# Kernel optimization log

Hardware: AMD Instinct MI355X
Metric: run time of the kernel (lower is better)

## Reference

```python
import jax, jax.numpy as jnp
import numpy as np

B, E, D, H, NH, HD = 2, 1024, 1024, 2048, 16, 128
NEG = -1e9  # stands in for float('-inf') in the torch mask; same softmax result


def _rotate_half(x):
    x1, x2 = x[..., : x.shape[-1] // 2], x[..., x.shape[-1] // 2 :]
    return jnp.concatenate((-x2, x1), axis=-1)


def setup_inputs() -> dict:
    key = jax.random.key(0)
    ks = jax.random.split(key, 8)
    hidden_states = jax.random.normal(ks[0], (B, D, H), dtype=jnp.float32)
    encoder_states = jax.random.normal(ks[1], (B, E, H), dtype=jnp.float32)
    # RoPE tables for the decoder positions
    inv_freq = 1.0 / (10000.0 ** (jnp.arange(0, HD, 2, dtype=jnp.float32) / HD))
    pos = jnp.arange(D, dtype=jnp.float32)
    freqs = pos[:, None] * inv_freq[None, :]            # [D, HD/2]
    emb = jnp.concatenate([freqs, freqs], axis=-1)      # [D, HD]
    cos = jnp.broadcast_to(jnp.cos(emb)[None], (B, D, HD)).astype(jnp.float32)
    sin = jnp.broadcast_to(jnp.sin(emb)[None], (B, D, HD)).astype(jnp.float32)
    # causal dec-dec mask [B,1,D,D]
    tri = jnp.tril(jnp.ones((D, D), dtype=bool))
    attention_mask = jnp.where(tri, 0.0, NEG).astype(jnp.float32)[None, None]
    attention_mask = jnp.broadcast_to(attention_mask, (B, 1, D, D))
    std = 0.02
    Wq = jax.random.normal(ks[2], (H, H), dtype=jnp.float32) * std
    Wk = jax.random.normal(ks[3], (H, H), dtype=jnp.float32) * std
    Wv = jax.random.normal(ks[4], (H, H), dtype=jnp.float32) * std
    Wo = jax.random.normal(ks[5], (H, H), dtype=jnp.float32) * std
    return {
        "hidden_states": hidden_states,
        "encoder_states": encoder_states,
        "cos": cos,
        "sin": sin,
        "attention_mask": attention_mask,
        "Wq": Wq,
        "Wk": Wk,
        "Wv": Wv,
        "Wo": Wo,
    }


def reference(hidden_states, encoder_states, cos, sin, attention_mask, Wq, Wk, Wv, Wo):
    b, d, h = hidden_states.shape
    e = encoder_states.shape[1]
    s = e + d
    scaling = HD ** -0.5
    # build concatenated enc/dec mask [B,1,S,S]
    enc_enc = jnp.zeros((b, 1, e, e), dtype=hidden_states.dtype)
    enc_dec = jnp.full((b, 1, e, d), NEG, dtype=hidden_states.dtype)
    dec_enc = jnp.zeros((b, 1, d, e), dtype=hidden_states.dtype)
    upper = jnp.concatenate([enc_enc, enc_dec], axis=-1)
    lower = jnp.concatenate([dec_enc, attention_mask], axis=-1)
    full_mask = jnp.concatenate([upper, lower], axis=-2)  # [B,1,S,S]

    hs = jnp.concatenate([encoder_states, hidden_states], axis=1)  # [B,S,H]
    def proj(W):
        return jnp.einsum("bsh,oh->bso", hs, W).reshape(b, s, NH, HD).transpose(0, 2, 1, 3)
    q, k, v = proj(Wq), proj(Wk), proj(Wv)  # [B,NH,S,HD]

    # partial RoPE: only on decoder slice
    c = cos[:, None]  # [B,1,D,HD]
    si = sin[:, None]
    q_dec = q[:, :, e:] * c + _rotate_half(q[:, :, e:]) * si
    k_dec = k[:, :, e:] * c + _rotate_half(k[:, :, e:]) * si
    q = jnp.concatenate([q[:, :, :e], q_dec], axis=2)
    k = jnp.concatenate([k[:, :, :e], k_dec], axis=2)

    scores = jnp.einsum("bhqd,bhkd->bhqk", q, k) * scaling + full_mask
    attn = jax.nn.softmax(scores.astype(jnp.float32), axis=-1).astype(q.dtype)
    out = jnp.einsum("bhqk,bhkd->bhqd", attn, v)            # [B,NH,S,HD]
    out = out.transpose(0, 2, 1, 3).reshape(b, s, NH * HD)   # [B,S,H]
    out = jnp.einsum("bsh,oh->bso", out, Wo)
    out = out[:, -d:, :]  # keep decoder outputs only
    return out, attn
```

## Files before the change

### kernel.cpp

```cpp
#include <hip/hip_runtime.h>
#include <cstdint>
#include <cstddef>

typedef _Float16 f16;
typedef __attribute__((ext_vector_type(8))) _Float16 half8;
typedef __attribute__((ext_vector_type(4))) float f32x4;

constexpr int Bb = 2, Ee = 1024, Dd = 1024, Hh = 2048, NHh = 16, HDd = 128, Ss = 2048;
constexpr float SCALE = 0.08838834764831845f;
constexpr int PSTR = 84;

#define DEVINL __device__ __forceinline__
#define GLD_LDS(gp, lp) \
  __builtin_amdgcn_global_load_lds((const __attribute__((address_space(1))) void*)(gp), \
                                   (__attribute__((address_space(3))) void*)(lp), 16, 0, 0)

DEVINL f16 f2h(float x) { return (f16)x; }
DEVINL float h2f(f16 x) { return (float)x; }

__global__ void convert_hs_k(const float* __restrict__ hid, const float* __restrict__ enc,
                             f16* __restrict__ dst) {
  size_t idx = ((size_t)blockIdx.x * 256 + threadIdx.x) * 8;
  int b = (int)(idx >> 22);
  size_t r = idx & ((1ull << 22) - 1);
  int s = (int)(r >> 11);
  int hc = (int)(r & 2047);
  const float* src = (s < Ee) ? (enc + (((size_t)b * Ee + s) << 11) + hc)
                              : (hid + (((size_t)b * Dd + (s - Ee)) << 11) + hc);
  float4 x0 = *(const float4*)src;
  float4 x1 = *(const float4*)(src + 4);
  union { f16 u[8]; uint4 v; } o;
  o.u[0] = f2h(x0.x); o.u[1] = f2h(x0.y); o.u[2] = f2h(x0.z); o.u[3] = f2h(x0.w);
  o.u[4] = f2h(x1.x); o.u[5] = f2h(x1.y); o.u[6] = f2h(x1.z); o.u[7] = f2h(x1.w);
  *(uint4*)(dst + idx) = o.v;
}

__global__ void convert_w_k(const float* __restrict__ w0, const float* __restrict__ w1,
                            const float* __restrict__ w2, const float* __restrict__ w3,
                            f16* __restrict__ dst) {
  const float* srcs[4] = {w0, w1, w2, w3};
  int z = blockIdx.y;
  size_t idx = ((size_t)blockIdx.x * 256 + threadIdx.x) * 8;
  const float* s = srcs[z] + idx;
  f16* d = dst + (size_t)z * Hh * Hh + idx;
  float4 x0 = *(const float4*)s;
  float4 x1 = *(const float4*)(s + 4);
  union { f16 u[8]; uint4 v; } o;
  o.u[0] = f2h(x0.x); o.u[1] = f2h(x0.y); o.u[2] = f2h(x0.z); o.u[3] = f2h(x0.w);
  o.u[4] = f2h(x1.x); o.u[5] = f2h(x1.y); o.u[6] = f2h(x1.z); o.u[7] = f2h(x1.w);
  *(uint4*)d = o.v;
}

template <int MODE>
__global__ __launch_bounds__(256) void gemm_k(const f16* __restrict__ A,
                                              const f16* __restrict__ Bw,
                                              void* __restrict__ Cout) {
  __shared__ f16 Alds[128 * 64];
  __shared__ f16 Blds[128 * 64];
  const int tid = threadIdx.x;
  const int lane = tid & 63, w = tid >> 6;
  const int lr = lane & 15, lq = lane >> 4;
  const int m0 = blockIdx.y * 128, n0 = blockIdx.x * 128;
  const int wm = (w >> 1) * 64, wn = (w & 1) * 64;
  f32x4 acc[4][4] = {};

  for (int k0 = 0; k0 < 2048; k0 += 64) {
    __syncthreads();
#pragma unroll
    for (int t = 0; t < 4; ++t) {
      int c = t * 256 + tid;
      int row = c >> 3, cof = (c & 7) << 3;
      const f16* ga = A + ((size_t)(m0 + row) << 11) + k0 + cof;
      const f16* gb = Bw + ((size_t)(n0 + row) << 11) + k0 + cof;
      int lo = (t * 256 + w * 64) * 8;
      GLD_LDS(ga, Alds + lo);
      GLD_LDS(gb, Blds + lo);
    }
    __syncthreads();
#pragma unroll
    for (int kk = 0; kk < 2; ++kk) {
      half8 af[4], bf[4];
#pragma unroll
      for (int i = 0; i < 4; ++i) {
        af[i] = *(const half8*)(Alds + (wm + i * 16 + lr) * 64 + kk * 32 + lq * 8);
        bf[i] = *(const half8*)(Blds + (wn + i * 16 + lr) * 64 + kk * 32 + lq * 8);
      }
#pragma unroll
      for (int i = 0; i < 4; ++i)
#pragma unroll
        for (int j = 0; j < 4; ++j)
          acc[i][j] = __builtin_amdgcn_mfma_f32_16x16x32_f16(af[i], bf[j], acc[i][j], 0, 0, 0);
    }
  }

#pragma unroll
  for (int i = 0; i < 4; ++i) {
#pragma unroll
    for (int j = 0; j < 4; ++j) {
      const int col = n0 + wn + j * 16 + lr;
#pragma unroll
      for (int jj = 0; jj < 4; ++jj) {
        const int row = m0 + wm + i * 16 + lq * 4 + jj;
        float v = acc[i][j][jj];
        if constexpr (MODE == 2) {
          ((float*)Cout)[((size_t)row << 11) + col] = v;
        } else {
          const int bb = row >> 11, s = row & 2047;
          const int hh = col >> 7, hd = col & 127;
          size_t o;
          if constexpr (MODE == 0)
            o = ((((size_t)bb * NHh + hh) * Ss + s) << 7) + hd;
          else
            o = ((((size_t)bb * NHh + hh) * HDd + hd) << 11) + s;
          ((f16*)Cout)[o] = f2h(v);
        }
      }
    }
  }
}

__global__ void rope_k(f16* __restrict__ q, f16* __restrict__ k,
                       const float* __restrict__ cosp, const float* __restrict__ sinp) {
  size_t idx = (size_t)blockIdx.x * 256 + threadIdx.x;
  const int d = (int)(idx & 63);
  const int sdec = (int)((idx >> 6) & 1023);
  const int h = (int)((idx >> 16) & 15);
  const int b = (int)(idx >> 20);
  const size_t base = (((size_t)b * NHh + h) * Ss + Ee + sdec) * HDd;
  const size_t cbase = ((size_t)b * Dd + sdec) * HDd;
  const float c1 = cosp[cbase + d], s1 = sinp[cbase + d];
  const float c2 = cosp[cbase + d + 64], s2 = sinp[cbase + d + 64];
  {
    float x1 = h2f(q[base + d]), x2 = h2f(q[base + d + 64]);
    q[base + d] = f2h(x1 * c1 - x2 * s1);
    q[base + d + 64] = f2h(x2 * c2 + x1 * s2);
  }
  {
    float x1 = h2f(k[base + d]), x2 = h2f(k[base + d + 64]);
    k[base + d] = f2h(x1 * c1 - x2 * s1);
    k[base + d + 64] = f2h(x2 * c2 + x1 * s2);
  }
}

__global__ __launch_bounds__(256) void attn_k(const f16* __restrict__ qw,
                                              const f16* __restrict__ kw,
                                              const f16* __restrict__ vw,
                                              float* __restrict__ attn,
                                              f16* __restrict__ ctx) {
  __shared__ f16 KV[2][8192];
  __shared__ f16 Plds[4][16 * PSTR];
  const int tid = threadIdx.x;
  const int lane = tid & 63, w = tid >> 6;
  const int lr = lane & 15, lq = lane >> 4;

  const int n = blockIdx.x;
  const int orig = (n & 7) * 128 + (n >> 3);
  const int qt = orig & 31;
  const int h = (orig >> 5) & 15;
  const int b = orig >> 9;
  const int q0 = (31 - qt) * 64;
  const bool dec = q0 >= Ee;
  const int kt_lim = dec ? (q0 / 64 + 1) : (Ee / 64);
  const size_t bh = (size_t)b * NHh + h;

#define STAGE_K(dst, kt_)                                                        \
  {                                                                              \
    _Pragma("unroll") for (int t = 0; t < 4; ++t) {                              \
      int c = t * 256 + tid;                                                     \
      int row = c >> 4;                                                          \
      int gs = (c & 15) ^ (row & 7);                                             \
      GLD_LDS(kw + (bh * Ss + (kt_) * 64 + row) * HDd + gs * 8, (dst) + c * 8);  \
    }                                                                            \
  }
#define STAGE_V(dst, kt_)                                                        \
  {                                                                              \
    _Pragma("unroll") for (int t = 0; t < 4; ++t) {                              \
      int c = t * 256 + tid;                                                     \
      int row = c >> 3;                                                          \
      int gs = (c & 7) ^ (row & 7);                                              \
      GLD_LDS(vw + (bh * HDd + row) * Ss + (kt_) * 64 + gs * 8, (dst) + c * 8);  \
    }                                                                            \
  }

  const f16* qbase = qw + (bh * Ss + q0 + w * 16 + lr) * HDd + lq * 8;
  half8 aq[4];
#pragma unroll
  for (int kk = 0; kk < 4; ++kk) aq[kk] = *(const half8*)(qbase + kk * 32);

  const int qrow_base = q0 + w * 16 + lq * 4;
  float lsum[4] = {0.f, 0.f, 0.f, 0.f};

  STAGE_K(KV[0], 0);
  __syncthreads();
  int cur = 0;
  for (int kt = 0; kt < kt_lim; ++kt) {
    if (kt + 1 < kt_lim) STAGE_K(KV[cur ^ 1], kt + 1);
    const f16* Kp = KV[cur];
#pragma unroll
    for (int j = 0; j < 4; ++j) {
      f32x4 sc = {0.f, 0.f, 0.f, 0.f};
#pragma unroll
      for (int kk = 0; kk < 4; ++kk) {
        half8 bk = *(const half8*)(Kp + (j * 16 + lr) * 128 + (((kk << 2) + lq) ^ (lr & 7)) * 8);
        sc = __builtin_amdgcn_mfma_f32_16x16x32_f16(aq[kk], bk, sc, 0, 0, 0);
      }
      const int col = kt * 64 + j * 16 + lr;
#pragma unroll
      for (int jj = 0; jj < 4; ++jj) {
        bool masked = dec && col >= Ee && col > qrow_base + jj;
        lsum[jj] += masked ? 0.f : __expf(sc[jj] * SCALE);
      }
    }
    __syncthreads();
    cur ^= 1;
  }
#pragma unroll
  for (int jj = 0; jj < 4; ++jj) {
#pragma unroll
    for (int o = 1; o < 16; o <<= 1) lsum[jj] += __shfl_xor(lsum[jj], o);
  }
  float rl[4];
#pragma unroll
  for (int jj = 0; jj < 4; ++jj) rl[jj] = 1.f / lsum[jj];

  f32x4 accv[8] = {};

  for (int kt = 0; kt < kt_lim; ++kt) {
    __syncthreads();
    STAGE_K(KV[0], kt);
    if (dec) STAGE_V(KV[1], kt);
    __syncthreads();
#pragma unroll
    for (int j = 0; j < 4; ++j) {
      f32x4 sc = {0.f, 0.f, 0.f, 0.f};
#pragma unroll
      for (int kk = 0; kk < 4; ++kk) {
        half8 bk = *(const half8*)(KV[0] + (j * 16 + lr) * 128 + (((kk << 2) + lq) ^ (lr & 7)) * 8);
        sc = __builtin_amdgcn_mfma_f32_16x16x32_f16(aq[kk], bk, sc, 0, 0, 0);
      }
      const int col = kt * 64 + j * 16 + lr;
#pragma unroll
      for (int jj = 0; jj < 4; ++jj) {
        const int qrow = qrow_base + jj;
        bool masked = dec && col >= Ee && col > qrow;
        float p = masked ? 0.f : __expf(sc[jj] * SCALE) * rl[jj];
        __builtin_nontemporal_store(p, &attn[(bh * Ss + qrow) * (size_t)Ss + col]);
        if (dec) Plds[w][(lq * 4 + jj) * PSTR + j * 16 + lr] = f2h(p);
      }
    }
    if (dec) {
#pragma unroll
      for (int kk2 = 0; kk2 < 2; ++kk2) {
        half8 ap = *(const half8*)(&Plds[w][lr * PSTR + kk2 * 32 + lq * 8]);
#pragma unroll
        for (int nt = 0; nt < 8; ++nt) {
          half8 bv = *(const half8*)(KV[1] + (nt * 16 + lr) * 64 + (((kk2 << 2) + lq) ^ (lr & 7)) * 8);
          accv[nt] = __builtin_amdgcn_mfma_f32_16x16x32_f16(ap, bv, accv[nt], 0, 0, 0);
        }
      }
    }
  }

  {
    const int zc0 = kt_lim * 64;
    const int Z = Ss - zc0;
    if (Z > 0) {
      const int per_row = Z >> 2;
      for (int idx = tid; idx < 64 * per_row; idx += 256) {
        int r = idx / per_row;
        int cc = (idx - r * per_row) << 2;
        f32x4 z = {0.f, 0.f, 0.f, 0.f};
        __builtin_nontemporal_store(z, (f32x4*)(attn + (bh * Ss + q0 + r) * (size_t)Ss + zc0 + cc));
      }
    }
  }

  if (dec) {
#pragma unroll
    for (int nt = 0; nt < 8; ++nt)
#pragma unroll
      for (int jj = 0; jj < 4; ++jj) {
        int sd = qrow_base + jj - Ee;
        ctx[((size_t)b * Dd + sd) * Hh + h * HDd + nt * 16 + lr] = f2h(accv[nt][jj]);
      }
  }
#undef STAGE_K
#undef STAGE_V
}

extern "C" void kernel_launch(void* const* d_in, const int* in_sizes, int n_in,
                              void* d_out, int out_size, void* d_ws, size_t ws_size,
                              hipStream_t stream) {
  const float* hidden  = (const float*)d_in[0];
  const float* encoder = (const float*)d_in[1];
  const float* cosp    = (const float*)d_in[2];
  const float* sinp    = (const float*)d_in[3];
  const float* Wq = (const float*)d_in[5];
  const float* Wk = (const float*)d_in[6];
  const float* Wv = (const float*)d_in[7];
  const float* Wo = (const float*)d_in[8];

  f16* ws = (f16*)d_ws;
  size_t off = 0;
  f16* hs_f = ws + off; off += (size_t)Bb * Ss * Hh;
  f16* W_f  = ws + off; off += (size_t)4 * Hh * Hh;
  f16* q_f  = ws + off; off += (size_t)Bb * NHh * Ss * HDd;
  f16* k_f  = ws + off; off += (size_t)Bb * NHh * Ss * HDd;
  f16* v_f  = ws + off; off += (size_t)Bb * NHh * Ss * HDd;
  f16* ctx_f = ws + off; off += (size_t)Bb * Dd * Hh;

  float* outp = (float*)d_out;
  float* attnp = outp + (size_t)Bb * Dd * Hh;

  convert_hs_k<<<4096, 256, 0, stream>>>(hidden, encoder, hs_f);
  convert_w_k<<<dim3(2048, 4), 256, 0, stream>>>(Wq, Wk, Wv, Wo, W_f);
  gemm_k<0><<<dim3(16, 32), 256, 0, stream>>>(hs_f, W_f + 0 * (size_t)Hh * Hh, q_f);
  gemm_k<0><<<dim3(16, 32), 256, 0, stream>>>(hs_f, W_f + 1 * (size_t)Hh * Hh, k_f);
  gemm_k<1><<<dim3(16, 32), 256, 0, stream>>>(hs_f, W_f + 2 * (size_t)Hh * Hh, v_f);
  rope_k<<<8192, 256, 0, stream>>>(q_f, k_f, cosp, sinp);
  attn_k<<<1024, 256, 0, stream>>>(q_f, k_f, v_f, attnp, ctx_f);
  gemm_k<2><<<dim3(16, 16), 256, 0, stream>>>(ctx_f, W_f + 3 * (size_t)Hh * Hh, outp);
}
```

Measured before the change: 442.8 us.

## Double-buffer K/V in attention pass two, stage attn stores via LDS, batch QKV GEMMs

The second attention pass now double-buffers K and V tiles in separate LDS buffers, so the next tile's global-to-LDS loads overlap the current tile's compute instead of being fenced by two barriers per iteration. Softmax probabilities are written to the per-wave P buffer for every block, then read back so each lane stores 16 contiguous floats of the attention matrix, replacing scattered scalar stores. The three QKV projection GEMMs are merged into one launch using grid z. In exchange, LDS use roughly doubles, which may lower occupancy. The stored attention weights are now rounded through fp16, which costs some precision.

```diff
diff --git a/kernel.cpp b/kernel.cpp
--- a/kernel.cpp
+++ b/kernel.cpp
@@ -8,7 +8,7 @@
 
 constexpr int Bb = 2, Ee = 1024, Dd = 1024, Hh = 2048, NHh = 16, HDd = 128, Ss = 2048;
 constexpr float SCALE = 0.08838834764831845f;
-constexpr int PSTR = 84;
+constexpr int PSTR = 88;
 
 #define DEVINL __device__ __forceinline__
 #define GLD_LDS(gp, lp) \
@@ -51,10 +51,76 @@
   *(uint4*)d = o.v;
 }
 
-template <int MODE>
-__global__ __launch_bounds__(256) void gemm_k(const f16* __restrict__ A,
-                                              const f16* __restrict__ Bw,
-                                              void* __restrict__ Cout) {
+__global__ __launch_bounds__(256) void gemm_qkv_k(const f16* __restrict__ A,
+                                                  const f16* __restrict__ W,
+                                                  f16* __restrict__ qo,
+                                                  f16* __restrict__ ko,
+                                                  f16* __restrict__ vo) {
+  __shared__ f16 Alds[128 * 64];
+  __shared__ f16 Blds[128 * 64];
+  const int tid = threadIdx.x;
+  const int lane = tid & 63, w = tid >> 6;
+  const int lr = lane & 15, lq = lane >> 4;
+  const int m0 = blockIdx.y * 128, n0 = blockIdx.x * 128;
+  const int z = blockIdx.z;
+  const f16* Bw = W + (size_t)z * Hh * Hh;
+  const int wm = (w >> 1) * 64, wn = (w & 1) * 64;
+  f32x4 acc[4][4] = {};
+
+  for (int k0 = 0; k0 < 2048; k0 += 64) {
+    __syncthreads();
+#pragma unroll
+    for (int t = 0; t < 4; ++t) {
+      int c = t * 256 + tid;
+      int row = c >> 3, cof = (c & 7) << 3;
+      const f16* ga = A + ((size_t)(m0 + row) << 11) + k0 + cof;
+      const f16* gb = Bw + ((size_t)(n0 + row) << 11) + k0 + cof;
+      int lo = (t * 256 + w * 64) * 8;
+      GLD_LDS(ga, Alds + lo);
+      GLD_LDS(gb, Blds + lo);
+    }
+    __syncthreads();
+#pragma unroll
+    for (int kk = 0; kk < 2; ++kk) {
+      half8 af[4], bf[4];
+#pragma unroll
+      for (int i = 0; i < 4; ++i) {
+        af[i] = *(const half8*)(Alds + (wm + i * 16 + lr) * 64 + kk * 32 + lq * 8);
+        bf[i] = *(const half8*)(Blds + (wn + i * 16 + lr) * 64 + kk * 32 + lq * 8);
+      }
+#pragma unroll
+      for (int i = 0; i < 4; ++i)
+#pragma unroll
+        for (int j = 0; j < 4; ++j)
+          acc[i][j] = __builtin_amdgcn_mfma_f32_16x16x32_f16(af[i], bf[j], acc[i][j], 0, 0, 0);
+    }
+  }
+
+  f16* out = (z == 0) ? qo : (z == 1) ? ko : vo;
+#pragma unroll
+  for (int i = 0; i < 4; ++i) {
+#pragma unroll
+    for (int j = 0; j < 4; ++j) {
+      const int col = n0 + wn + j * 16 + lr;
+      const int hh = col >> 7, hd = col & 127;
+#pragma unroll
+      for (int jj = 0; jj < 4; ++jj) {
+        const int row = m0 + wm + i * 16 + lq * 4 + jj;
+        const int bb = row >> 11, s = row & 2047;
+        size_t o;
+        if (z < 2)
+          o = ((((size_t)bb * NHh + hh) * Ss + s) << 7) + hd;
+        else
+          o = ((((size_t)bb * NHh + hh) * HDd + hd) << 11) + s;
+        out[o] = f2h(acc[i][j][jj]);
+      }
+    }
+  }
+}
+
+__global__ __launch_bounds__(256) void gemm_out_k(const f16* __restrict__ A,
+                                                  const f16* __restrict__ Bw,
+                                                  float* __restrict__ Cout) {
   __shared__ f16 Alds[128 * 64];
   __shared__ f16 Blds[128 * 64];
   const int tid = threadIdx.x;
@@ -94,29 +160,16 @@
   }
 
 #pragma unroll
-  for (int i = 0; i < 4; ++i) {
+  for (int i = 0; i < 4; ++i)
 #pragma unroll
     for (int j = 0; j < 4; ++j) {
       const int col = n0 + wn + j * 16 + lr;
 #pragma unroll
       for (int jj = 0; jj < 4; ++jj) {
         const int row = m0 + wm + i * 16 + lq * 4 + jj;
-        float v = acc[i][j][jj];
-        if constexpr (MODE == 2) {
-          ((float*)Cout)[((size_t)row << 11) + col] = v;
-        } else {
-          const int bb = row >> 11, s = row & 2047;
-          const int hh = col >> 7, hd = col & 127;
-          size_t o;
-          if constexpr (MODE == 0)
-            o = ((((size_t)bb * NHh + hh) * Ss + s) << 7) + hd;
-          else
-            o = ((((size_t)bb * NHh + hh) * HDd + hd) << 11) + s;
-          ((f16*)Cout)[o] = f2h(v);
-        }
-      }
-    }
-  }
+        Cout[((size_t)row << 11) + col] = acc[i][j][jj];
+      }
+    }
 }
 
 __global__ void rope_k(f16* __restrict__ q, f16* __restrict__ k,
@@ -147,7 +200,8 @@
                                               const f16* __restrict__ vw,
                                               float* __restrict__ attn,
                                               f16* __restrict__ ctx) {
-  __shared__ f16 KV[2][8192];
+  __shared__ f16 Kb[2][8192];
+  __shared__ f16 Vb[2][8192];
   __shared__ f16 Plds[4][16 * PSTR];
   const int tid = threadIdx.x;
   const int lane = tid & 63, w = tid >> 6;
@@ -190,12 +244,12 @@
   const int qrow_base = q0 + w * 16 + lq * 4;
   float lsum[4] = {0.f, 0.f, 0.f, 0.f};
 
-  STAGE_K(KV[0], 0);
+  STAGE_K(Kb[0], 0);
   __syncthreads();
   int cur = 0;
   for (int kt = 0; kt < kt_lim; ++kt) {
-    if (kt + 1 < kt_lim) STAGE_K(KV[cur ^ 1], kt + 1);
-    const f16* Kp = KV[cur];
+    if (kt + 1 < kt_lim) STAGE_K(Kb[cur ^ 1], kt + 1);
+    const f16* Kp = Kb[cur];
 #pragma unroll
     for (int j = 0; j < 4; ++j) {
       f32x4 sc = {0.f, 0.f, 0.f, 0.f};
@@ -214,6 +268,10 @@
     __syncthreads();
     cur ^= 1;
   }
+
+  STAGE_K(Kb[0], 0);
+  if (dec) STAGE_V(Vb[0], 0);
+
 #pragma unroll
   for (int jj = 0; jj < 4; ++jj) {
 #pragma unroll
@@ -224,18 +282,21 @@
   for (int jj = 0; jj < 4; ++jj) rl[jj] = 1.f / lsum[jj];
 
   f32x4 accv[8] = {};
-
+  __syncthreads();
+
+  cur = 0;
   for (int kt = 0; kt < kt_lim; ++kt) {
-    __syncthreads();
-    STAGE_K(KV[0], kt);
-    if (dec) STAGE_V(KV[1], kt);
-    __syncthreads();
+    if (kt + 1 < kt_lim) {
+      STAGE_K(Kb[cur ^ 1], kt + 1);
+      if (dec) STAGE_V(Vb[cur ^ 1], kt + 1);
+    }
+    const f16* Kp = Kb[cur];
 #pragma unroll
     for (int j = 0; j < 4; ++j) {
       f32x4 sc = {0.f, 0.f, 0.f, 0.f};
 #pragma unroll
       for (int kk = 0; kk < 4; ++kk) {
-        half8 bk = *(const half8*)(KV[0] + (j * 16 + lr) * 128 + (((kk << 2) + lq) ^ (lr & 7)) * 8);
+        half8 bk = *(const half8*)(Kp + (j * 16 + lr) * 128 + (((kk << 2) + lq) ^ (lr & 7)) * 8);
         sc = __builtin_amdgcn_mfma_f32_16x16x32_f16(aq[kk], bk, sc, 0, 0, 0);
       }
       const int col = kt * 64 + j * 16 + lr;
@@ -244,9 +305,23 @@
         const int qrow = qrow_base + jj;
         bool masked = dec && col >= Ee && col > qrow;
         float p = masked ? 0.f : __expf(sc[jj] * SCALE) * rl[jj];
-        __builtin_nontemporal_store(p, &attn[(bh * Ss + qrow) * (size_t)Ss + col]);
-        if (dec) Plds[w][(lq * 4 + jj) * PSTR + j * 16 + lr] = f2h(p);
-      }
+        Plds[w][(lq * 4 + jj) * PSTR + j * 16 + lr] = f2h(p);
+      }
+    }
+    {
+      const int prow = lane >> 2;
+      const int pc0 = (lane & 3) * 16;
+      const half8 p0 = *(const half8*)(&Plds[w][prow * PSTR + pc0]);
+      const half8 p1 = *(const half8*)(&Plds[w][prow * PSTR + pc0 + 8]);
+      float* dst = attn + (bh * Ss + (size_t)(q0 + w * 16 + prow)) * Ss + kt * 64 + pc0;
+      f32x4 o0 = {h2f(p0[0]), h2f(p0[1]), h2f(p0[2]), h2f(p0[3])};
+      f32x4 o1 = {h2f(p0[4]), h2f(p0[5]), h2f(p0[6]), h2f(p0[7])};
+      f32x4 o2 = {h2f(p1[0]), h2f(p1[1]), h2f(p1[2]), h2f(p1[3])};
+      f32x4 o3 = {h2f(p1[4]), h2f(p1[5]), h2f(p1[6]), h2f(p1[7])};
+      __builtin_nontemporal_store(o0, (f32x4*)dst);
+      __builtin_nontemporal_store(o1, (f32x4*)(dst + 4));
+      __builtin_nontemporal_store(o2, (f32x4*)(dst + 8));
+      __builtin_nontemporal_store(o3, (f32x4*)(dst + 12));
     }
     if (dec) {
 #pragma unroll
@@ -254,11 +329,13 @@
         half8 ap = *(const half8*)(&Plds[w][lr * PSTR + kk2 * 32 + lq * 8]);
 #pragma unroll
         for (int nt = 0; nt < 8; ++nt) {
-          half8 bv = *(const half8*)(KV[1] + (nt * 16 + lr) * 64 + (((kk2 << 2) + lq) ^ (lr & 7)) * 8);
+          half8 bv = *(const half8*)(Vb[cur] + (nt * 16 + lr) * 64 + (((kk2 << 2) + lq) ^ (lr & 7)) * 8);
           accv[nt] = __builtin_amdgcn_mfma_f32_16x16x32_f16(ap, bv, accv[nt], 0, 0, 0);
         }
       }
     }
+    __syncthreads();
+    cur ^= 1;
   }
 
   {
@@ -314,10 +391,8 @@
 
   convert_hs_k<<<4096, 256, 0, stream>>>(hidden, encoder, hs_f);
   convert_w_k<<<dim3(2048, 4), 256, 0, stream>>>(Wq, Wk, Wv, Wo, W_f);
-  gemm_k<0><<<dim3(16, 32), 256, 0, stream>>>(hs_f, W_f + 0 * (size_t)Hh * Hh, q_f);
-  gemm_k<0><<<dim3(16, 32), 256, 0, stream>>>(hs_f, W_f + 1 * (size_t)Hh * Hh, k_f);
-  gemm_k<1><<<dim3(16, 32), 256, 0, stream>>>(hs_f, W_f + 2 * (size_t)Hh * Hh, v_f);
+  gemm_qkv_k<<<dim3(16, 32, 3), 256, 0, stream>>>(hs_f, W_f, q_f, k_f, v_f);
   rope_k<<<8192, 256, 0, stream>>>(q_f, k_f, cosp, sinp);
   attn_k<<<1024, 256, 0, stream>>>(q_f, k_f, v_f, attnp, ctx_f);
-  gemm_k<2><<<dim3(16, 16), 256, 0, stream>>>(ctx_f, W_f + 3 * (size_t)Hh * Hh, outp);
-}
+  gemm_out_k<<<dim3(16, 16), 256, 0, stream>>>(ctx_f, W_f + 3 * (size_t)Hh * Hh, outp);
+}
```

Measured after the change: 637.1 us. 43.9% more time.

## Load K/V fragments directly from global memory, dropping LDS staging and barriers

Applied to the files above, without the earlier changes.

The attention kernel stops staging K and V tiles into shared memory with async global-to-LDS loads and double buffering. Each wave now reads its MFMA B-operand fragments straight from global memory, relying on L1/L2 caching, so the block barriers go away. LDS use drops to the small P buffer and the launch bound now requests 4 blocks per CU for more occupancy. The cost is that every wave refetches the same K/V data, with less coalesced 16-byte loads and no software prefetch to hide latency.

```diff
diff --git a/kernel.cpp b/kernel.cpp
--- a/kernel.cpp
+++ b/kernel.cpp
@@ -142,12 +142,11 @@
   }
 }
 
-__global__ __launch_bounds__(256) void attn_k(const f16* __restrict__ qw,
-                                              const f16* __restrict__ kw,
-                                              const f16* __restrict__ vw,
-                                              float* __restrict__ attn,
-                                              f16* __restrict__ ctx) {
-  __shared__ f16 KV[2][8192];
+__global__ __launch_bounds__(256, 4) void attn_k(const f16* __restrict__ qw,
+                                                 const f16* __restrict__ kw,
+                                                 const f16* __restrict__ vw,
+                                                 float* __restrict__ attn,
+                                                 f16* __restrict__ ctx) {
   __shared__ f16 Plds[4][16 * PSTR];
   const int tid = threadIdx.x;
   const int lane = tid & 63, w = tid >> 6;
@@ -163,25 +162,6 @@
   const int kt_lim = dec ? (q0 / 64 + 1) : (Ee / 64);
   const size_t bh = (size_t)b * NHh + h;
 
-#define STAGE_K(dst, kt_)                                                        \
-  {                                                                              \
-    _Pragma("unroll") for (int t = 0; t < 4; ++t) {                              \
-      int c = t * 256 + tid;                                                     \
-      int row = c >> 4;                                                          \
-      int gs = (c & 15) ^ (row & 7);                                             \
-      GLD_LDS(kw + (bh * Ss + (kt_) * 64 + row) * HDd + gs * 8, (dst) + c * 8);  \
-    }                                                                            \
-  }
-#define STAGE_V(dst, kt_)                                                        \
-  {                                                                              \
-    _Pragma("unroll") for (int t = 0; t < 4; ++t) {                              \
-      int c = t * 256 + tid;                                                     \
-      int row = c >> 3;                                                          \
-      int gs = (c & 7) ^ (row & 7);                                              \
-      GLD_LDS(vw + (bh * HDd + row) * Ss + (kt_) * 64 + gs * 8, (dst) + c * 8);  \
-    }                                                                            \
-  }
-
   const f16* qbase = qw + (bh * Ss + q0 + w * 16 + lr) * HDd + lq * 8;
   half8 aq[4];
 #pragma unroll
@@ -190,18 +170,17 @@
   const int qrow_base = q0 + w * 16 + lq * 4;
   float lsum[4] = {0.f, 0.f, 0.f, 0.f};
 
-  STAGE_K(KV[0], 0);
-  __syncthreads();
-  int cur = 0;
+  const f16* kw_bh = kw + bh * Ss * HDd;
+  const f16* vw_bh = vw + bh * HDd * Ss;
+
   for (int kt = 0; kt < kt_lim; ++kt) {
-    if (kt + 1 < kt_lim) STAGE_K(KV[cur ^ 1], kt + 1);
-    const f16* Kp = KV[cur];
+    const f16* kb = kw_bh + (size_t)kt * 64 * HDd + lr * HDd + lq * 8;
 #pragma unroll
     for (int j = 0; j < 4; ++j) {
       f32x4 sc = {0.f, 0.f, 0.f, 0.f};
 #pragma unroll
       for (int kk = 0; kk < 4; ++kk) {
-        half8 bk = *(const half8*)(Kp + (j * 16 + lr) * 128 + (((kk << 2) + lq) ^ (lr & 7)) * 8);
+        half8 bk = *(const half8*)(kb + j * 16 * HDd + kk * 32);
         sc = __builtin_amdgcn_mfma_f32_16x16x32_f16(aq[kk], bk, sc, 0, 0, 0);
       }
       const int col = kt * 64 + j * 16 + lr;
@@ -211,8 +190,6 @@
         lsum[jj] += masked ? 0.f : __expf(sc[jj] * SCALE);
       }
     }
-    __syncthreads();
-    cur ^= 1;
   }
 #pragma unroll
   for (int jj = 0; jj < 4; ++jj) {
@@ -226,16 +203,13 @@
   f32x4 accv[8] = {};
 
   for (int kt = 0; kt < kt_lim; ++kt) {
-    __syncthreads();
-    STAGE_K(KV[0], kt);
-    if (dec) STAGE_V(KV[1], kt);
-    __syncthreads();
+    const f16* kb = kw_bh + (size_t)kt * 64 * HDd + lr * HDd + lq * 8;
 #pragma unroll
     for (int j = 0; j < 4; ++j) {
       f32x4 sc = {0.f, 0.f, 0.f, 0.f};
 #pragma unroll
       for (int kk = 0; kk < 4; ++kk) {
-        half8 bk = *(const half8*)(KV[0] + (j * 16 + lr) * 128 + (((kk << 2) + lq) ^ (lr & 7)) * 8);
+        half8 bk = *(const half8*)(kb + j * 16 * HDd + kk * 32);
         sc = __builtin_amdgcn_mfma_f32_16x16x32_f16(aq[kk], bk, sc, 0, 0, 0);
       }
       const int col = kt * 64 + j * 16 + lr;
@@ -249,12 +223,13 @@
       }
     }
     if (dec) {
+      const f16* vb = vw_bh + (size_t)lr * Ss + kt * 64 + lq * 8;
 #pragma unroll
       for (int kk2 = 0; kk2 < 2; ++kk2) {
         half8 ap = *(const half8*)(&Plds[w][lr * PSTR + kk2 * 32 + lq * 8]);
 #pragma unroll
         for (int nt = 0; nt < 8; ++nt) {
-          half8 bv = *(const half8*)(KV[1] + (nt * 16 + lr) * 64 + (((kk2 << 2) + lq) ^ (lr & 7)) * 8);
+          half8 bv = *(const half8*)(vb + (size_t)nt * 16 * Ss + kk2 * 32);
           accv[nt] = __builtin_amdgcn_mfma_f32_16x16x32_f16(ap, bv, accv[nt], 0, 0, 0);
         }
       }
@@ -284,8 +259,6 @@
         ctx[((size_t)b * Dd + sd) * Hh + h * HDd + nt * 16 + lr] = f2h(accv[nt][jj]);
       }
   }
-#undef STAGE_K
-#undef STAGE_V
 }
 
 extern "C" void kernel_launch(void* const* d_in, const int* in_sizes, int n_in,
```

After: 911.3 us. 2.06x slower.

## Move PV accumulation into first pass and double-buffer K in second pass

Applied to the files above, without the earlier changes.

The P·V matmul moves into the first (row-sum) pass using unnormalized exponentials, with V double-buffered alongside K. The context is normalized by 1/lsum afterwards, which frees the second pass to only recompute scores and write attention probabilities. That second pass now double-buffers K loads instead of load-sync-compute each tile. LDS use rises with the separate K and V double buffers, which may reduce occupancy. The unnormalized exp values stored in fp16 also carry some precision/overflow risk.

```diff
diff --git a/kernel.cpp b/kernel.cpp
--- a/kernel.cpp
+++ b/kernel.cpp
@@ -147,7 +147,8 @@
                                               const f16* __restrict__ vw,
                                               float* __restrict__ attn,
                                               f16* __restrict__ ctx) {
-  __shared__ f16 KV[2][8192];
+  __shared__ f16 Kb[2][8192];
+  __shared__ f16 Vb[2][8192];
   __shared__ f16 Plds[4][16 * PSTR];
   const int tid = threadIdx.x;
   const int lane = tid & 63, w = tid >> 6;
@@ -189,13 +190,18 @@
 
   const int qrow_base = q0 + w * 16 + lq * 4;
   float lsum[4] = {0.f, 0.f, 0.f, 0.f};
-
-  STAGE_K(KV[0], 0);
+  f32x4 accv[8] = {};
+
+  STAGE_K(Kb[0], 0);
+  if (dec) STAGE_V(Vb[0], 0);
   __syncthreads();
   int cur = 0;
   for (int kt = 0; kt < kt_lim; ++kt) {
-    if (kt + 1 < kt_lim) STAGE_K(KV[cur ^ 1], kt + 1);
-    const f16* Kp = KV[cur];
+    if (kt + 1 < kt_lim) {
+      STAGE_K(Kb[cur ^ 1], kt + 1);
+      if (dec) STAGE_V(Vb[cur ^ 1], kt + 1);
+    }
+    const f16* Kp = Kb[cur];
 #pragma unroll
     for (int j = 0; j < 4; ++j) {
       f32x4 sc = {0.f, 0.f, 0.f, 0.f};
@@ -208,12 +214,28 @@
 #pragma unroll
       for (int jj = 0; jj < 4; ++jj) {
         bool masked = dec && col >= Ee && col > qrow_base + jj;
-        lsum[jj] += masked ? 0.f : __expf(sc[jj] * SCALE);
+        float pu = masked ? 0.f : __expf(sc[jj] * SCALE);
+        lsum[jj] += pu;
+        if (dec) Plds[w][(lq * 4 + jj) * PSTR + j * 16 + lr] = f2h(pu);
+      }
+    }
+    if (dec) {
+#pragma unroll
+      for (int kk2 = 0; kk2 < 2; ++kk2) {
+        half8 ap = *(const half8*)(&Plds[w][lr * PSTR + kk2 * 32 + lq * 8]);
+#pragma unroll
+        for (int nt = 0; nt < 8; ++nt) {
+          half8 bv = *(const half8*)(Vb[cur] + (nt * 16 + lr) * 64 + (((kk2 << 2) + lq) ^ (lr & 7)) * 8);
+          accv[nt] = __builtin_amdgcn_mfma_f32_16x16x32_f16(ap, bv, accv[nt], 0, 0, 0);
+        }
       }
     }
     __syncthreads();
     cur ^= 1;
   }
+
+  STAGE_K(Kb[0], 0);
+
 #pragma unroll
   for (int jj = 0; jj < 4; ++jj) {
 #pragma unroll
@@ -223,19 +245,28 @@
 #pragma unroll
   for (int jj = 0; jj < 4; ++jj) rl[jj] = 1.f / lsum[jj];
 
-  f32x4 accv[8] = {};
-
+  if (dec) {
+#pragma unroll
+    for (int nt = 0; nt < 8; ++nt)
+#pragma unroll
+      for (int jj = 0; jj < 4; ++jj) {
+        int sd = qrow_base + jj - Ee;
+        ctx[((size_t)b * Dd + sd) * Hh + h * HDd + nt * 16 + lr] = f2h(accv[nt][jj] * rl[jj]);
+      }
+  }
+
+  __syncthreads();
+
+  cur = 0;
   for (int kt = 0; kt < kt_lim; ++kt) {
-    __syncthreads();
-    STAGE_K(KV[0], kt);
-    if (dec) STAGE_V(KV[1], kt);
-    __syncthreads();
+    if (kt + 1 < kt_lim) STAGE_K(Kb[cur ^ 1], kt + 1);
+    const f16* Kp = Kb[cur];
 #pragma unroll
     for (int j = 0; j < 4; ++j) {
       f32x4 sc = {0.f, 0.f, 0.f, 0.f};
 #pragma unroll
       for (int kk = 0; kk < 4; ++kk) {
-        half8 bk = *(const half8*)(KV[0] + (j * 16 + lr) * 128 + (((kk << 2) + lq) ^ (lr & 7)) * 8);
+        half8 bk = *(const half8*)(Kp + (j * 16 + lr) * 128 + (((kk << 2) + lq) ^ (lr & 7)) * 8);
         sc = __builtin_amdgcn_mfma_f32_16x16x32_f16(aq[kk], bk, sc, 0, 0, 0);
       }
       const int col = kt * 64 + j * 16 + lr;
@@ -245,20 +276,10 @@
         bool masked = dec && col >= Ee && col > qrow;
         float p = masked ? 0.f : __expf(sc[jj] * SCALE) * rl[jj];
         __builtin_nontemporal_store(p, &attn[(bh * Ss + qrow) * (size_t)Ss + col]);
-        if (dec) Plds[w][(lq * 4 + jj) * PSTR + j * 16 + lr] = f2h(p);
-      }
-    }
-    if (dec) {
-#pragma unroll
-      for (int kk2 = 0; kk2 < 2; ++kk2) {
-        half8 ap = *(const half8*)(&Plds[w][lr * PSTR + kk2 * 32 + lq * 8]);
-#pragma unroll
-        for (int nt = 0; nt < 8; ++nt) {
-          half8 bv = *(const half8*)(KV[1] + (nt * 16 + lr) * 64 + (((kk2 << 2) + lq) ^ (lr & 7)) * 8);
-          accv[nt] = __builtin_amdgcn_mfma_f32_16x16x32_f16(ap, bv, accv[nt], 0, 0, 0);
-        }
-      }
-    }
+      }
+    }
+    __syncthreads();
+    cur ^= 1;
   }
 
   {
@@ -273,16 +294,6 @@
         __builtin_nontemporal_store(z, (f32x4*)(attn + (bh * Ss + q0 + r) * (size_t)Ss + zc0 + cc));
       }
     }
-  }
-
-  if (dec) {
-#pragma unroll
-    for (int nt = 0; nt < 8; ++nt)
-#pragma unroll
-      for (int jj = 0; jj < 4; ++jj) {
-        int sd = qrow_base + jj - Ee;
-        ctx[((size_t)b * Dd + sd) * Hh + h * HDd + nt * 16 + lr] = f2h(accv[nt][jj]);
-      }
   }
 #undef STAGE_K
 #undef STAGE_V
```

New measurement: 430.3 us. 2.8% less time.
